# Performance work log

Measured on AMD Instinct MI355X. Metric: run time of the kernel, lower is better.

Reference implementation:

```python
import jax, jax.numpy as jnp
import numpy as np

T, B, V, L = 512, 32, 8000, 100
BLANK = 0
NEG = -1e30  # safe -inf surrogate


def setup_inputs() -> dict:
    key = jax.random.key(0)
    k1, k2 = jax.random.split(key)
    acts = jax.random.normal(k1, (T, B, V), dtype=jnp.float32)
    # non-blank labels in [1, V)
    targets = jax.random.randint(k2, (B, L), 1, V, dtype=jnp.int32)
    act_lens = jnp.full((B,), T, dtype=jnp.int32)
    label_lens = jnp.full((B,), L, dtype=jnp.int32)
    return {"acts": acts, "targets": targets, "act_lens": act_lens, "label_lens": label_lens}


def _ctc_loss(acts, targets, act_lens, label_lens):
    Tt, Bb, Vv = acts.shape
    Ll = targets.shape[1]
    S = 2 * Ll + 1
    # warp-ctc applies log-softmax to the raw activations internally
    logp = jax.nn.log_softmax(acts, axis=-1)  # [T,B,V]
    # extended label sequence: blank interleaved (blank at even indices)
    ext = jnp.zeros((Bb, S), jnp.int32).at[:, 1::2].set(targets.astype(jnp.int32))
    # emission log-probs gathered per extended label: [T,B,S]
    lp_ext = jnp.take_along_axis(logp, jnp.broadcast_to(ext[None], (Tt, Bb, S)), axis=2)
    ext_m2 = jnp.pad(ext[:, :-2], ((0, 0), (2, 0)), constant_values=-1)
    can_skip = (ext != BLANK) & (ext != ext_m2)  # [B,S]

    alpha0 = jnp.full((Bb, S), NEG, acts.dtype)
    alpha0 = alpha0.at[:, 0].set(lp_ext[0, :, 0]).at[:, 1].set(lp_ext[0, :, 1])

    def step(alpha, xs):
        lp_t, t = xs
        a1 = alpha
        a2 = jnp.pad(alpha[:, :-1], ((0, 0), (1, 0)), constant_values=NEG)
        a3 = jnp.where(can_skip, jnp.pad(alpha[:, :-2], ((0, 0), (2, 0)), constant_values=NEG), NEG)
        new = jnp.logaddexp(a1, jnp.logaddexp(a2, a3)) + lp_t
        active = (t < act_lens)[:, None]  # freeze alpha past each sample's length
        return jnp.where(active, new, alpha), None

    alpha, _ = jax.lax.scan(step, alpha0, (lp_ext[1:], jnp.arange(1, Tt)))
    b = jnp.arange(Bb)
    s_last = 2 * label_lens  # final blank position per sample
    ll = jnp.logaddexp(alpha[b, s_last], alpha[b, s_last - 1])
    per_sample = -ll
    return jnp.sum(per_sample) / Bb  # size_average=True, length_average=False


def reference(acts, targets, act_lens, label_lens):
    return _ctc_loss(acts, targets, act_lens, label_lens)
```

## Files before the change

kernel.cpp:

```cpp
#include <hip/hip_runtime.h>
#include <hip/hip_bf16.h>


#define LOG2E 1.4426950408889634f
#define LN2   0.69314718055994530942f
#define NEGS  (-1.4426950408889634e30f)

__device__ __forceinline__ float lae2(float a, float b) {
    float m = fmaxf(a, b);
    float d = fminf(a, b) - m;
    return m + log2f(1.0f + exp2f(d));
}
__device__ __forceinline__ float lae3(float a, float b, float c) {
    float m = fmaxf(fmaxf(a, b), c);
    float s = exp2f(a - m) + exp2f(b - m) + exp2f(c - m);
    return m + log2f(s);
}

__global__ __launch_bounds__(256)
void ctc_rowlse(const float* __restrict__ acts, const int* __restrict__ targets,
                float* __restrict__ lp) {
    const int B = 32, V = 8000, L = 100, RS = 104;
    const int bid = blockIdx.x;
    const int t = bid >> 5, b = bid & 31;
    const int tid = threadIdx.x;

    __shared__ float red[8];

    const float* rowp = acts + ((size_t)t * B + b) * V;
    const float4* g = (const float4*)rowp;

    float4 v[8];
    #pragma unroll
    for (int j = 0; j < 8; ++j) {
        int idx = tid + j * 256;
        if (j < 7 || tid < 208) v[j] = g[idx];
        else v[j] = make_float4(-3.0e38f, -3.0e38f, -3.0e38f, -3.0e38f);
    }

    float m = -3.0e38f;
    #pragma unroll
    for (int j = 0; j < 8; ++j)
        m = fmaxf(m, fmaxf(fmaxf(v[j].x, v[j].y), fmaxf(v[j].z, v[j].w)));
    #pragma unroll
    for (int o = 32; o > 0; o >>= 1) m = fmaxf(m, __shfl_xor(m, o));
    if ((tid & 63) == 0) red[tid >> 6] = m;
    __syncthreads();
    m = fmaxf(fmaxf(red[0], red[1]), fmaxf(red[2], red[3]));

    float s = 0.f;
    #pragma unroll
    for (int j = 0; j < 8; ++j) {
        s += exp2f((v[j].x - m) * LOG2E) + exp2f((v[j].y - m) * LOG2E)
           + exp2f((v[j].z - m) * LOG2E) + exp2f((v[j].w - m) * LOG2E);
    }
    #pragma unroll
    for (int o = 32; o > 0; o >>= 1) s += __shfl_xor(s, o);
    if ((tid & 63) == 0) red[4 + (tid >> 6)] = s;
    __syncthreads();
    s = red[4] + red[5] + red[6] + red[7];

    const float base = m * LOG2E + log2f(s);

    if (tid < 101) {
        int cls = (tid == 0) ? 0 : targets[b * L + tid - 1];
        lp[((size_t)b * 512 + t) * RS + tid] = rowp[cls] * LOG2E - base;
    }
}

__global__ __launch_bounds__(64)
void ctc_alpha(const float* __restrict__ lp, const int* __restrict__ targets,
               const int* __restrict__ act_lens, const int* __restrict__ label_lens,
               float* __restrict__ partials) {
    const int T = 512, L = 100, RS = 104, CH = 32;
    const int b = blockIdx.x;
    const int l = threadIdx.x;

    __shared__ float4 buf[2][CH * RS / 4];
    __shared__ float afin[256];

    const int* tg = targets + b * L;

    const int s0 = 4 * l;
    const int i1 = 2 * l;
    const int i3 = 2 * l + 1;
    const bool v1 = (s0 + 1) <= 200;
    const bool v3 = (s0 + 3) <= 200;
    const int q1  = (i1 < L) ? i1 : (L - 1);
    const int q1m = (i1 >= 1) ? ((i1 - 1 < L) ? i1 - 1 : (L - 1)) : 0;
    const int q3  = (i3 < L) ? i3 : (L - 1);
    const int c1 = tg[q1], c1m = tg[q1m], c3 = tg[q3];
    const bool can1 = (i1 == 0) || (c1 != c1m);
    const bool can3 = (c3 != c1);
    const int k1 = v1 ? (1 + i1) : 0;
    const int k3 = v3 ? (1 + i3) : 0;
    const int act_len = act_lens[b];

    const float4* gsrc = (const float4*)(lp + (size_t)b * T * RS);

    float4 stg[13];
    #pragma unroll
    for (int i = 0; i < 13; ++i) stg[i] = gsrc[i * 64 + l];
    #pragma unroll
    for (int i = 0; i < 13; ++i) buf[0][i * 64 + l] = stg[i];
    __syncthreads();

    float a0 = NEGS, a1 = NEGS, a2 = NEGS, a3 = NEGS;
    {
        const float* row0 = (const float*)&buf[0][0];
        if (l == 0) { a0 = row0[0]; a1 = row0[1]; }
    }

    int gt = 1;
    for (int c = 0; c < 16; ++c) {
        if (c < 15) {
            const float4* gn = gsrc + (size_t)(c + 1) * (CH * RS / 4);
            #pragma unroll
            for (int i = 0; i < 13; ++i) stg[i] = gn[i * 64 + l];
        }
        const float* rowbase = (const float*)&buf[c & 1][0];
        const int tstart = (c == 0) ? 1 : 0;
        for (int tt = tstart; tt < CH; ++tt, ++gt) {
            const float* row = rowbase + tt * RS;
            float lpB = row[0];
            float lq1 = v1 ? row[k1] : NEGS;
            float lq3 = v3 ? row[k3] : NEGS;
            float p3 = __shfl_up(a3, 1);
            if (l == 0) p3 = NEGS;
            float na0 = lae2(a0, p3) + lpB;
            float na1 = lae3(a1, a0, can1 ? p3 : NEGS) + lq1;
            float na2 = lae2(a2, a1) + lpB;
            float na3 = lae3(a3, a2, can3 ? a1 : NEGS) + lq3;
            if (gt < act_len) { a0 = na0; a1 = na1; a2 = na2; a3 = na3; }
        }
        if (c < 15) {
            float4* dst = &buf[(c + 1) & 1][0];
            #pragma unroll
            for (int i = 0; i < 13; ++i) dst[i * 64 + l] = stg[i];
            __syncthreads();
        }
    }

    afin[4 * l + 0] = a0; afin[4 * l + 1] = a1;
    afin[4 * l + 2] = a2; afin[4 * l + 3] = a3;
    __syncthreads();
    if (l == 0) {
        int Lb = label_lens[b];
        int sl = 2 * Lb;
        float ll = lae2(afin[sl], afin[sl - 1]);
        partials[b] = -ll * LN2;
    }
}

__global__ __launch_bounds__(64)
void ctc_final(const float* __restrict__ partials, float* __restrict__ out) {
    int tid = threadIdx.x;
    float v = (tid < 32) ? partials[tid] : 0.f;
    #pragma unroll
    for (int o = 32; o > 0; o >>= 1) v += __shfl_xor(v, o);
    if (tid == 0) out[0] = v * (1.0f / 32.0f);
}

extern "C" void kernel_launch(void* const* d_in, const int* in_sizes, int n_in,
                              void* d_out, int out_size, void* d_ws, size_t ws_size,
                              hipStream_t stream) {
    const float* acts      = (const float*)d_in[0];
    const int*   targets   = (const int*)d_in[1];
    const int*   act_lens  = (const int*)d_in[2];
    const int*   label_lens= (const int*)d_in[3];

    float* lp       = (float*)d_ws;
    float* partials = (float*)((char*)d_ws + (size_t)32 * 512 * 104 * sizeof(float));

    ctc_rowlse<<<16384, 256, 0, stream>>>(acts, targets, lp);
    ctc_alpha <<<32, 64, 0, stream>>>(lp, targets, act_lens, label_lens, partials);
    ctc_final <<<1, 64, 0, stream>>>(partials, (float*)d_out);
}
```

Before: 824.1 us.

## Fuse log-softmax and alpha recursion into one producer-consumer kernel with atomic counters

Merges the row log-softmax kernel, the alpha recursion and the final reduction into one launch. The first 32 blocks are consumers that spin on per-(batch, 32-timestep chunk) atomic counters, so the serial alpha recursion starts while producer blocks are still computing later timesteps. This is meant to hide most of the latency of the serial recursion behind the bandwidth-bound softmax pass and to remove two launches. The last consumer to finish reduces the partials itself. The risk is that correctness depends on the 32 consumer blocks being resident and on producers being scheduled roughly in chunk order, and the consumer blocks now use 256 threads with only 64 doing the recursion.

After: 1.474 ms. +78.8%, slower.

```diff
diff --git a/kernel.cpp b/kernel.cpp
--- a/kernel.cpp
+++ b/kernel.cpp
@@ -5,6 +5,7 @@
 #define LOG2E 1.4426950408889634f
 #define LN2   0.69314718055994530942f
 #define NEGS  (-1.4426950408889634e30f)
+#define RS 112
 
 __device__ __forceinline__ float lae2(float a, float b) {
     float m = fmaxf(a, b);
@@ -17,162 +18,172 @@
     return m + log2f(s);
 }
 
+__global__ __launch_bounds__(512)
+void ctc_zero(int* __restrict__ cnt2, int* __restrict__ done) {
+    int i = threadIdx.x;
+    cnt2[i] = 0;
+    if (i == 0) *done = 0;
+}
+
 __global__ __launch_bounds__(256)
-void ctc_rowlse(const float* __restrict__ acts, const int* __restrict__ targets,
-                float* __restrict__ lp) {
-    const int B = 32, V = 8000, L = 100, RS = 104;
-    const int bid = blockIdx.x;
-    const int t = bid >> 5, b = bid & 31;
+void ctc_fused(const float* __restrict__ acts, const int* __restrict__ targets,
+               const int* __restrict__ act_lens, const int* __restrict__ label_lens,
+               float* __restrict__ lp, float* __restrict__ partials,
+               int* __restrict__ cnt2, int* __restrict__ done,
+               float* __restrict__ out) {
+    const int B = 32, V = 8000, L = 100;
     const int tid = threadIdx.x;
 
-    __shared__ float red[8];
+    if (blockIdx.x >= 32) {
+        const int pbid = (int)blockIdx.x - 32;
+        const int t = pbid >> 5, b = pbid & 31;
+        __shared__ float red[8];
 
-    const float* rowp = acts + ((size_t)t * B + b) * V;
-    const float4* g = (const float4*)rowp;
+        const float* rowp = acts + ((size_t)t * B + b) * V;
+        const float4* g = (const float4*)rowp;
 
-    float4 v[8];
-    #pragma unroll
-    for (int j = 0; j < 8; ++j) {
-        int idx = tid + j * 256;
-        if (j < 7 || tid < 208) v[j] = g[idx];
-        else v[j] = make_float4(-3.0e38f, -3.0e38f, -3.0e38f, -3.0e38f);
-    }
+        float gval = 0.f;
+        if (tid < 101) {
+            int cls = (tid == 0) ? 0 : targets[b * L + tid - 1];
+            gval = rowp[cls];
+        }
 
-    float m = -3.0e38f;
-    #pragma unroll
-    for (int j = 0; j < 8; ++j)
-        m = fmaxf(m, fmaxf(fmaxf(v[j].x, v[j].y), fmaxf(v[j].z, v[j].w)));
-    #pragma unroll
-    for (int o = 32; o > 0; o >>= 1) m = fmaxf(m, __shfl_xor(m, o));
-    if ((tid & 63) == 0) red[tid >> 6] = m;
-    __syncthreads();
-    m = fmaxf(fmaxf(red[0], red[1]), fmaxf(red[2], red[3]));
+        float4 v[8];
+        #pragma unroll
+        for (int j = 0; j < 8; ++j) {
+            int idx = tid + j * 256;
+            if (j < 7 || tid < 208) v[j] = g[idx];
+            else v[j] = make_float4(-3.0e38f, -3.0e38f, -3.0e38f, -3.0e38f);
+        }
 
-    float s = 0.f;
-    #pragma unroll
-    for (int j = 0; j < 8; ++j) {
-        s += exp2f((v[j].x - m) * LOG2E) + exp2f((v[j].y - m) * LOG2E)
-           + exp2f((v[j].z - m) * LOG2E) + exp2f((v[j].w - m) * LOG2E);
-    }
-    #pragma unroll
-    for (int o = 32; o > 0; o >>= 1) s += __shfl_xor(s, o);
-    if ((tid & 63) == 0) red[4 + (tid >> 6)] = s;
-    __syncthreads();
-    s = red[4] + red[5] + red[6] + red[7];
+        float m = -3.0e38f;
+        #pragma unroll
+        for (int j = 0; j < 8; ++j)
+            m = fmaxf(m, fmaxf(fmaxf(v[j].x, v[j].y), fmaxf(v[j].z, v[j].w)));
+        #pragma unroll
+        for (int o = 32; o > 0; o >>= 1) m = fmaxf(m, __shfl_xor(m, o));
+        if ((tid & 63) == 0) red[tid >> 6] = m;
+        __syncthreads();
+        m = fmaxf(fmaxf(red[0], red[1]), fmaxf(red[2], red[3]));
 
-    const float base = m * LOG2E + log2f(s);
+        float s = 0.f;
+        #pragma unroll
+        for (int j = 0; j < 8; ++j) {
+            s += exp2f((v[j].x - m) * LOG2E) + exp2f((v[j].y - m) * LOG2E)
+               + exp2f((v[j].z - m) * LOG2E) + exp2f((v[j].w - m) * LOG2E);
+        }
+        #pragma unroll
+        for (int o = 32; o > 0; o >>= 1) s += __shfl_xor(s, o);
+        if ((tid & 63) == 0) red[4 + (tid >> 6)] = s;
+        __syncthreads();
+        s = red[4] + red[5] + red[6] + red[7];
 
-    if (tid < 101) {
-        int cls = (tid == 0) ? 0 : targets[b * L + tid - 1];
-        lp[((size_t)b * 512 + t) * RS + tid] = rowp[cls] * LOG2E - base;
-    }
-}
+        const float base = m * LOG2E + log2f(s);
+        if (tid < 101)
+            lp[((size_t)b * 512 + t) * RS + tid] = gval * LOG2E - base;
 
-__global__ __launch_bounds__(64)
-void ctc_alpha(const float* __restrict__ lp, const int* __restrict__ targets,
-               const int* __restrict__ act_lens, const int* __restrict__ label_lens,
-               float* __restrict__ partials) {
-    const int T = 512, L = 100, RS = 104, CH = 32;
-    const int b = blockIdx.x;
-    const int l = threadIdx.x;
+        __syncthreads();
+        if (tid == 0)
+            __hip_atomic_fetch_add(&cnt2[b * 16 + (t >> 5)], 1,
+                                   __ATOMIC_RELEASE, __HIP_MEMORY_SCOPE_AGENT);
+    } else {
+        const int b = (int)blockIdx.x;
+        const int l = tid;
+        __shared__ float4 buf4[896];
+        __shared__ float afin[256];
+        __shared__ int lastflag;
 
-    __shared__ float4 buf[2][CH * RS / 4];
-    __shared__ float afin[256];
+        const int* tg = targets + b * L;
+        const int i1 = 2 * l;
+        const int i3 = 2 * l + 1;
+        const bool v1 = (4 * l + 1) <= 200;
+        const bool v3 = (4 * l + 3) <= 200;
+        const int q1  = (i1 < L) ? i1 : (L - 1);
+        const int q1m = (i1 >= 1) ? ((i1 - 1 < L) ? i1 - 1 : (L - 1)) : 0;
+        const int q3  = (i3 < L) ? i3 : (L - 1);
+        const int c1 = tg[q1], c1m = tg[q1m], c3 = tg[q3];
+        const bool can1 = (i1 == 0) || (c1 != c1m);
+        const bool can3 = (c3 != c1);
+        const int k1 = v1 ? (1 + i1) : 0;
+        const int k3 = v3 ? (1 + i3) : 0;
+        const int act_len = act_lens[b];
 
-    const int* tg = targets + b * L;
+        float a0 = NEGS, a1 = NEGS, a2 = NEGS, a3 = NEGS;
 
-    const int s0 = 4 * l;
-    const int i1 = 2 * l;
-    const int i3 = 2 * l + 1;
-    const bool v1 = (s0 + 1) <= 200;
-    const bool v3 = (s0 + 3) <= 200;
-    const int q1  = (i1 < L) ? i1 : (L - 1);
-    const int q1m = (i1 >= 1) ? ((i1 - 1 < L) ? i1 - 1 : (L - 1)) : 0;
-    const int q3  = (i3 < L) ? i3 : (L - 1);
-    const int c1 = tg[q1], c1m = tg[q1m], c3 = tg[q3];
-    const bool can1 = (i1 == 0) || (c1 != c1m);
-    const bool can3 = (c3 != c1);
-    const int k1 = v1 ? (1 + i1) : 0;
-    const int k3 = v3 ? (1 + i3) : 0;
-    const int act_len = act_lens[b];
+        for (int c = 0; c < 16; ++c) {
+            if (tid == 0) {
+                while (__hip_atomic_load(&cnt2[b * 16 + c], __ATOMIC_RELAXED,
+                                         __HIP_MEMORY_SCOPE_AGENT) < 32)
+                    __builtin_amdgcn_s_sleep(2);
+                while (__hip_atomic_load(&cnt2[b * 16 + c], __ATOMIC_ACQUIRE,
+                                         __HIP_MEMORY_SCOPE_AGENT) < 32)
+                    __builtin_amdgcn_s_sleep(1);
+            }
+            __syncthreads();
 
-    const float4* gsrc = (const float4*)(lp + (size_t)b * T * RS);
+            const float4* gsrc = (const float4*)(lp + ((size_t)b * 512 + c * 32) * RS);
+            for (int i = tid; i < 896; i += 256) buf4[i] = gsrc[i];
+            __syncthreads();
 
-    float4 stg[13];
-    #pragma unroll
-    for (int i = 0; i < 13; ++i) stg[i] = gsrc[i * 64 + l];
-    #pragma unroll
-    for (int i = 0; i < 13; ++i) buf[0][i * 64 + l] = stg[i];
-    __syncthreads();
+            if (tid < 64) {
+                const float* rowbase = (const float*)buf4;
+                if (c == 0 && l == 0) { a0 = rowbase[0]; a1 = rowbase[1]; }
+                const int tstart = (c == 0) ? 1 : 0;
+                for (int tt = tstart; tt < 32; ++tt) {
+                    const float* row = rowbase + tt * RS;
+                    float lpB = row[0];
+                    float lq1 = v1 ? row[k1] : NEGS;
+                    float lq3 = v3 ? row[k3] : NEGS;
+                    float p3 = __shfl_up(a3, 1);
+                    if (l == 0) p3 = NEGS;
+                    float na0 = lae2(a0, p3) + lpB;
+                    float na1 = lae3(a1, a0, can1 ? p3 : NEGS) + lq1;
+                    float na2 = lae2(a2, a1) + lpB;
+                    float na3 = lae3(a3, a2, can3 ? a1 : NEGS) + lq3;
+                    if (c * 32 + tt < act_len) { a0 = na0; a1 = na1; a2 = na2; a3 = na3; }
+                }
+            }
+        }
 
-    float a0 = NEGS, a1 = NEGS, a2 = NEGS, a3 = NEGS;
-    {
-        const float* row0 = (const float*)&buf[0][0];
-        if (l == 0) { a0 = row0[0]; a1 = row0[1]; }
-    }
-
-    int gt = 1;
-    for (int c = 0; c < 16; ++c) {
-        if (c < 15) {
-            const float4* gn = gsrc + (size_t)(c + 1) * (CH * RS / 4);
+        if (tid < 64) {
+            afin[4 * l + 0] = a0; afin[4 * l + 1] = a1;
+            afin[4 * l + 2] = a2; afin[4 * l + 3] = a3;
+        }
+        __syncthreads();
+        if (tid == 0) {
+            int Lb = label_lens[b];
+            int sl = 2 * Lb;
+            float ll = lae2(afin[sl], afin[sl - 1]);
+            partials[b] = -ll * LN2;
+            int old = __hip_atomic_fetch_add(done, 1, __ATOMIC_ACQ_REL,
+                                             __HIP_MEMORY_SCOPE_AGENT);
+            lastflag = (old == 31) ? 1 : 0;
+        }
+        __syncthreads();
+        if (lastflag && tid < 64) {
+            float vv = (tid < 32) ? partials[tid] : 0.f;
             #pragma unroll
-            for (int i = 0; i < 13; ++i) stg[i] = gn[i * 64 + l];
-        }
-        const float* rowbase = (const float*)&buf[c & 1][0];
-        const int tstart = (c == 0) ? 1 : 0;
-        for (int tt = tstart; tt < CH; ++tt, ++gt) {
-            const float* row = rowbase + tt * RS;
-            float lpB = row[0];
-            float lq1 = v1 ? row[k1] : NEGS;
-            float lq3 = v3 ? row[k3] : NEGS;
-            float p3 = __shfl_up(a3, 1);
-            if (l == 0) p3 = NEGS;
-            float na0 = lae2(a0, p3) + lpB;
-            float na1 = lae3(a1, a0, can1 ? p3 : NEGS) + lq1;
-            float na2 = lae2(a2, a1) + lpB;
-            float na3 = lae3(a3, a2, can3 ? a1 : NEGS) + lq3;
-            if (gt < act_len) { a0 = na0; a1 = na1; a2 = na2; a3 = na3; }
-        }
-        if (c < 15) {
-            float4* dst = &buf[(c + 1) & 1][0];
-            #pragma unroll
-            for (int i = 0; i < 13; ++i) dst[i * 64 + l] = stg[i];
-            __syncthreads();
+            for (int o = 32; o > 0; o >>= 1) vv += __shfl_xor(vv, o);
+            if (tid == 0) out[0] = vv * (1.0f / 32.0f);
         }
     }
-
-    afin[4 * l + 0] = a0; afin[4 * l + 1] = a1;
-    afin[4 * l + 2] = a2; afin[4 * l + 3] = a3;
-    __syncthreads();
-    if (l == 0) {
-        int Lb = label_lens[b];
-        int sl = 2 * Lb;
-        float ll = lae2(afin[sl], afin[sl - 1]);
-        partials[b] = -ll * LN2;
-    }
-}
-
-__global__ __launch_bounds__(64)
-void ctc_final(const float* __restrict__ partials, float* __restrict__ out) {
-    int tid = threadIdx.x;
-    float v = (tid < 32) ? partials[tid] : 0.f;
-    #pragma unroll
-    for (int o = 32; o > 0; o >>= 1) v += __shfl_xor(v, o);
-    if (tid == 0) out[0] = v * (1.0f / 32.0f);
 }
 
 extern "C" void kernel_launch(void* const* d_in, const int* in_sizes, int n_in,
                               void* d_out, int out_size, void* d_ws, size_t ws_size,
                               hipStream_t stream) {
-    const float* acts      = (const float*)d_in[0];
-    const int*   targets   = (const int*)d_in[1];
-    const int*   act_lens  = (const int*)d_in[2];
-    const int*   label_lens= (const int*)d_in[3];
+    const float* acts       = (const float*)d_in[0];
+    const int*   targets    = (const int*)d_in[1];
+    const int*   act_lens   = (const int*)d_in[2];
+    const int*   label_lens = (const int*)d_in[3];
 
-    float* lp       = (float*)d_ws;
-    float* partials = (float*)((char*)d_ws + (size_t)32 * 512 * 104 * sizeof(float));
+    char* w = (char*)d_ws;
+    float* lp       = (float*)w;
+    float* partials = (float*)(w + 7340032);
+    int*   cnt2     = (int*)  (w + 7340032 + 128);
+    int*   done     = (int*)  (w + 7340032 + 128 + 2048);
 
-    ctc_rowlse<<<16384, 256, 0, stream>>>(acts, targets, lp);
-    ctc_alpha <<<32, 64, 0, stream>>>(lp, targets, act_lens, label_lens, partials);
-    ctc_final <<<1, 64, 0, stream>>>(partials, (float*)d_out);
+    ctc_zero <<<1, 512, 0, stream>>>(cnt2, done);
+    ctc_fused<<<16416, 256, 0, stream>>>(acts, targets, act_lens, label_lens,
+                                         lp, partials, cnt2, done, (float*)d_out);
 }
```
